# Optimization experiments

Measured on AMD Instinct MI355X. Metric: run time of the kernel, lower is better.

The kernel has to match this reference:

```python
import jax, jax.numpy as jnp
import numpy as np
jax.config.update("jax_enable_x64", True)

K = 10            # num_digits
NUM_CLASSES = 10  # digit classes 0..9
EQ_TOKEN = 28
PRIMES = np.array([7, 11, 13, 17, 19, 23, 29, 31, 37], dtype=np.int64)
TWO_PI = 2.0 * np.pi
M_TOTAL = int(np.prod(PRIMES.astype(object)))  # product of primes ~2.47e11 (needs int64)
_crt = []
for p in PRIMES:
    Mi = M_TOTAL // int(p)
    _crt.append((Mi * pow(Mi, -1, int(p))) % M_TOTAL)
CRT_C = jnp.array(_crt, dtype=jnp.int64)                 # [P] CRT mixing coefficients
POW10 = jnp.array([[pow(10, k, int(p)) for k in range(K)] for p in PRIMES], dtype=jnp.float32)  # [P,K]
PR_F = jnp.array(PRIMES, dtype=jnp.float32)
PR_I = jnp.array(PRIMES, dtype=jnp.int64)
POW10_DEC = jnp.array([10 ** k for k in range(K)], dtype=jnp.int64)
_op = np.full(64, -1, dtype=np.int64)
_op[20:25] = np.arange(5)  # tokens 20..24 -> ops add,sub,mul,exp,div
OP_TABLE = jnp.array(_op)


def encode(d):
    # d [B,S,K] soft base-10 digits -> RNS circle encoding [B,S,P,2]
    theta = TWO_PI * jnp.einsum('bsk,pk->bsp', d, POW10) / PR_F
    return jnp.stack([jnp.cos(theta), jnp.sin(theta)], axis=-1)


def decode_residues(circle):
    # [B,S,P,2] -> integer residues mod p, [B,S,P] int64
    theta = jnp.arctan2(circle[..., 1], circle[..., 0])
    r = jnp.round(theta / TWO_PI * PR_F).astype(jnp.int64)
    return jnp.mod(r, PR_I)


def circle_add(a, b):
    ca, sa = a[..., 0], a[..., 1]
    cb, sb = b[..., 0], b[..., 1]
    return jnp.stack([ca * cb - sa * sb, sa * cb + ca * sb], axis=-1)


def circle_sub(a, b):
    ca, sa = a[..., 0], a[..., 1]
    cb, sb = b[..., 0], b[..., 1]
    return jnp.stack([ca * cb + sa * sb, sa * cb - ca * sb], axis=-1)


def modpow(base, exp, mod):
    # elementwise modular exponentiation, exponents < 64 (6 square-and-multiply steps)
    res = jnp.ones_like(base)
    b = jnp.mod(base, mod)
    e = exp
    for _ in range(6):
        res = jnp.where((e & 1) == 1, (res * b) % mod, res)
        b = (b * b) % mod
        e = e >> 1
    return res


def crt(residues):
    # CRT reconstruction: [B,S,P] -> [B,S] int64 in [0, M_TOTAL)
    return jnp.mod(jnp.sum(residues * CRT_C, axis=-1), M_TOTAL)


def crt_signed(residues):
    n = crt(residues)
    return jnp.where(n > M_TOTAL // 2, n - M_TOTAL, n)


def int_to_digits(n):
    # [B,S] int64 -> [B,S,K] float base-10 digits, LSB-first
    return ((n[..., None] // POW10_DEC) % 10).astype(jnp.float32)


def int_to_digits_signed(n):
    sign = (n < 0).astype(jnp.float32)[..., None]
    return jnp.concatenate([int_to_digits(jnp.abs(n)), sign], axis=-1)  # [B,S,K+1]


def decode_all_ops(a_c, b_c):
    # All 5 operations decoded to digit vectors -> [B,S,5K+1]
    ra = decode_residues(a_c)
    rb = decode_residues(b_c)
    add_d = int_to_digits(crt(decode_residues(circle_add(a_c, b_c))))
    sub_d = int_to_digits_signed(crt_signed(decode_residues(circle_sub(a_c, b_c))))
    mul_d = int_to_digits(crt((ra * rb) % PR_I))
    exp_d = int_to_digits(crt(modpow(ra, rb, PR_I)))
    inv = modpow(rb, PR_I - 2, PR_I)  # Fermat inverse
    div_r = jnp.where(rb == 0, 0, (ra * inv) % PR_I)
    div_d = int_to_digits(crt(div_r))
    return jnp.concatenate([add_d, sub_d, mul_d, exp_d, div_d], axis=-1)


def select_op(results, input_ids):
    # [B,S,5K+1] -> [B,S,K+1]: pick the relevant operation per sequence
    B, S, _ = results.shape
    pad = jnp.zeros((B, S, 1), results.dtype)
    ops = jnp.stack([
        jnp.concatenate([results[..., 0:K], pad], -1),
        results[..., K:2 * K + 1],
        jnp.concatenate([results[..., 2 * K + 1:3 * K + 1], pad], -1),
        jnp.concatenate([results[..., 3 * K + 1:4 * K + 1], pad], -1),
        jnp.concatenate([results[..., 4 * K + 1:5 * K + 1], pad], -1),
    ], axis=-2)  # [B,S,5,K+1]
    is_op = OP_TABLE[jnp.clip(input_ids, 0, 63)] >= 0
    op_pos = jnp.argmax(is_op, axis=1)  # first operator position per sequence
    op_tok = jnp.take_along_axis(input_ids, op_pos[:, None], axis=1)[:, 0]
    op_idx = OP_TABLE[jnp.clip(op_tok, 0, 63)]
    gidx = jnp.broadcast_to(jnp.clip(op_idx, 0, 4)[:, None, None, None], (B, S, 1, K + 1))
    sel = jnp.take_along_axis(ops, gidx, axis=-2)[..., 0, :]
    valid = (op_idx >= 0).astype(results.dtype)[:, None, None]
    return sel * valid


def reorder_msb(res):
    # LSB-first digits -> MSB-first, -1 sentinel past the last significant digit
    digits = res[..., :K]
    sign = res[..., K:]
    idx = jnp.arange(K)
    nz = digits != 0
    highest = jnp.max(jnp.where(nz, idx, -1), axis=-1)
    num_sig = jnp.where(jnp.any(nz, axis=-1), highest + 1, 1)
    src = jnp.clip(num_sig[..., None] - 1 - idx, 0, K - 1)
    msb = jnp.take_along_axis(digits, src, axis=-1)
    msb = jnp.where(idx < num_sig[..., None], msb, -1.0)
    return jnp.concatenate([msb, sign], axis=-1)


def setup_inputs() -> dict:
    key = jax.random.key(0)
    ks = jax.random.split(key, 6)
    B, S, D, MH = 16, 2048, 768, 128
    h = jax.random.normal(ks[0], (B, S, D), dtype=jnp.float32)
    input_ids = jax.random.randint(ks[1], (B, S), 0, 50, dtype=jnp.int64)
    W1 = jax.random.normal(ks[2], (D, MH), dtype=jnp.float32) * 0.02
    b1 = jnp.zeros((MH,), jnp.float32)
    W2 = jax.random.normal(ks[3], (MH, 2 * K * NUM_CLASSES), dtype=jnp.float32) * 0.02
    b2 = jnp.zeros((2 * K * NUM_CLASSES,), jnp.float32)
    Winj = jax.random.normal(ks[4], (K + 1, D), dtype=jnp.float32) * 0.001  # injector_init_std
    binj = jnp.zeros((D,), jnp.float32)
    gate_logit = jnp.array(-2.0, jnp.float32)  # gate_init_logit
    return {"h": h, "W1": W1, "b1": b1, "W2": W2, "b2": b2,
            "Winj": Winj, "binj": binj, "gate_logit": gate_logit, "input_ids": input_ids}


def reference(h, W1, b1, W2, b2, Winj, binj, gate_logit, input_ids):
    B, S, D = h.shape
    # OperandExtractor: per-token MLP -> soft digits for operands a and b
    hid = jax.nn.relu(h @ W1 + b1)
    logits = (hid @ W2 + b2).reshape(B, S, 2, K, NUM_CLASSES)
    probs = jax.nn.softmax(logits, axis=-1)
    dig = jnp.einsum('bsokc,c->bsok', probs, jnp.arange(NUM_CLASSES, dtype=h.dtype))
    d_a, d_b = dig[..., 0, :], dig[..., 1, :]
    # RNSCircleEncoder (frozen)
    a_c = encode(d_a)
    b_c = encode(d_b)
    # ArithmeticCompute + CRT decode: detached (torch.no_grad in original)
    results = jax.lax.stop_gradient(decode_all_ops(a_c, b_c).astype(h.dtype))
    sel = select_op(results, input_ids)
    msb = reorder_msb(sel)
    # ResultInjector: gated linear injection into the residual stream
    inj = msb @ Winj + binj
    h_prime = h + jax.nn.sigmoid(gate_logit) * inj
    # only inject for sequences containing the '=' token
    has_eq = jnp.any(input_ids == EQ_TOKEN, axis=1).astype(h.dtype)[:, None, None]
    h_prime = h + (h_prime - h) * has_eq
    return h_prime, d_a, d_b
```

## Files before the change

kernel.cpp:

```cpp
#include <hip/hip_runtime.h>

typedef unsigned short u16;
typedef unsigned int   u32;
typedef unsigned long long u64;

typedef __attribute__((ext_vector_type(8))) short short8;
typedef __attribute__((ext_vector_type(4))) float f32x4;

#define DEV static __device__ __forceinline__

__constant__ float POW10F[9][10] = {
  {1,3,2,6,4,5,1,3,2,6},
  {1,10,1,10,1,10,1,10,1,10},
  {1,10,9,12,3,4,1,10,9,12},
  {1,10,15,14,4,6,9,5,16,7},
  {1,10,5,12,6,3,11,15,17,18},
  {1,10,8,11,18,19,6,14,2,20},
  {1,10,13,14,24,8,22,17,25,18},
  {1,10,7,8,18,25,2,20,14,16},
  {1,10,26,1,10,26,1,10,26,1},
};

#define M_TOTAL  247357937827ull
#define M_HALF   123678968913ull

DEV u16 f2bf_rne(float f){
  u32 u = __float_as_uint(f);
  return (u16)((u + 0x7FFFu + ((u >> 16) & 1u)) >> 16);
}
DEV float bf2f(u16 v){ return __uint_as_float(((u32)v) << 16); }

DEV short8 pack_bf16(float4 a, float4 b){
  union { short8 s; u32 u[4]; } r;
  r.u[0] = (__float_as_uint(a.x) >> 16) | (__float_as_uint(a.y) & 0xFFFF0000u);
  r.u[1] = (__float_as_uint(a.z) >> 16) | (__float_as_uint(a.w) & 0xFFFF0000u);
  r.u[2] = (__float_as_uint(b.x) >> 16) | (__float_as_uint(b.y) & 0xFFFF0000u);
  r.u[3] = (__float_as_uint(b.z) >> 16) | (__float_as_uint(b.w) & 0xFFFF0000u);
  return r.s;
}

DEV void load_lds16(const void* g, void* l){
  __builtin_amdgcn_global_load_lds((const __attribute__((address_space(1))) void*)g,
                                   (__attribute__((address_space(3))) void*)l, 16, 0, 0);
}

DEV int modpow6(int b, int e, int p){
  int res = 1; b %= p;
  #pragma unroll
  for (int i = 0; i < 6; ++i){
    if (e & 1) res = (res * b) % p;
    b = (b * b) % p;
    e >>= 1;
  }
  return res;
}

__global__ void prelude_kernel(const int* __restrict__ ids, const float* __restrict__ W1,
                               const float* __restrict__ W2, int* __restrict__ op_idx,
                               float* __restrict__ has_eq, u16* __restrict__ w1f,
                               u16* __restrict__ w2f){
  __shared__ int smin[256];
  __shared__ int seq[256];
  int bid = blockIdx.x, tid = threadIdx.x;
  if (bid < 16){
    int b = bid;
    int best = 2048, eq = 0;
    for (int i = tid; i < 2048; i += 256){
      int t = ids[b * 2048 + i];
      if (t >= 20 && t < 25) best = min(best, i);
      eq |= (t == 28) ? 1 : 0;
    }
    smin[tid] = best; seq[tid] = eq;
    __syncthreads();
    for (int s = 128; s > 0; s >>= 1){
      if (tid < s){ smin[tid] = min(smin[tid], smin[tid + s]); seq[tid] |= seq[tid + s]; }
      __syncthreads();
    }
    if (tid == 0){
      int op = -1;
      if (smin[0] < 2048) op = ids[b * 2048 + smin[0]] - 20;
      op_idx[b] = op;
      has_eq[b] = seq[0] ? 1.0f : 0.0f;
    }
  } else {
    int t = (bid - 16) * 256 + tid;
    if (t < 12288){
      int blk = t >> 6, L = t & 63;
      int T = blk >> 3, b = blk & 7;
      int q = L >> 4, ln = L & 15;
      #pragma unroll
      for (int j = 0; j < 8; ++j){
        int k = 32 * T + 8 * q + j;
        int n = 16 * b + ln;
        w1f[(size_t)blk * 512 + L * 8 + j] = f2bf_rne(W1[k * 128 + n]);
      }
    } else {
      int t2 = t - 12288;
      int blk = t2 >> 6, L = t2 & 63;
      int ts = blk / 13, b2 = blk % 13;
      int q = L >> 4, ln = L & 15;
      #pragma unroll
      for (int j = 0; j < 8; ++j){
        int k = 32 * ts + 8 * q + j;
        int n = 16 * b2 + ln;
        w2f[(size_t)blk * 512 + L * 8 + j] = (n < 200) ? f2bf_rne(W2[k * 200 + n]) : (u16)0;
      }
    }
  }
}

__launch_bounds__(256, 2)
__global__ void mega_kernel(const float* __restrict__ h, const u16* __restrict__ w1f,
                            const u16* __restrict__ w2f, const float* __restrict__ b1,
                            const float* __restrict__ b2, const float* __restrict__ Winj,
                            const float* __restrict__ binj, const float* __restrict__ gate,
                            const int* __restrict__ op_idx_ws, const float* __restrict__ has_eq_ws,
                            float* __restrict__ dout){
  __shared__ __align__(16) char lds[49152];
  u16*   wbuf     = (u16*)lds;
  char*  tail     = lds + 32768;
  float* digits_s = (float*)tail;
  float* tab_s    = (float*)(tail + 5120);
  u64*   ops_s    = (u64*)(tail + 9728);
  float* msbv     = (float*)(tail + 12288);
  u16*   hidf     = (u16*)tail;
  float* winj_s   = (float*)lds;
  float* binj_s   = (float*)(lds + 33792);

  const int tid  = threadIdx.x;
  const int w    = tid >> 6;
  const int lane = tid & 63;
  const int ln   = lane & 15, q = lane >> 4;
  const int wg   = blockIdx.x;
  const int tok0 = wg * 64;
  const int gtok = tok0 + w * 16 + ln;
  const int batch = wg >> 5;

  const int   op = op_idx_ws[batch];
  const float G  = has_eq_ws[batch] * (1.0f / (1.0f + __expf(-gate[0])));

  float b1v[8];
  #pragma unroll
  for (int b = 0; b < 8; ++b) b1v[b] = b1[ln + 16 * b];
  float b2v[13];
  #pragma unroll
  for (int b = 0; b < 13; ++b){ int n = ln + 16 * b; b2v[b] = (n < 200) ? b2[n] : 0.0f; }

  f32x4 acc[8];
  #pragma unroll
  for (int b = 0; b < 8; ++b) acc[b] = (f32x4)0.0f;

  const float4* ap = (const float4*)(h + (size_t)gtok * 768);
  float4 xa[2], xb[2];
  #pragma unroll
  for (int i = 0; i < 4; ++i){
    int bl = w * 4 + i;
    load_lds16(w1f + (size_t)(((bl >> 3)) * 8 + (bl & 7)) * 512 + lane * 8,
               wbuf + bl * 512);
  }
  #pragma unroll
  for (int t = 0; t < 2; ++t){ xa[t] = ap[t * 8 + q * 2]; xb[t] = ap[t * 8 + q * 2 + 1]; }

  #pragma unroll
  for (int c = 0; c < 12; ++c){
    __syncthreads();
    const u16* cur = wbuf + (c & 1) * 8192;
    if (c < 11){
      u16* nxt = wbuf + ((c + 1) & 1) * 8192;
      #pragma unroll
      for (int i = 0; i < 4; ++i){
        int bl = w * 4 + i;
        int T  = (c + 1) * 2 + (bl >> 3);
        load_lds16(w1f + (size_t)(T * 8 + (bl & 7)) * 512 + lane * 8, nxt + bl * 512);
      }
    }
    short8 af[2];
    #pragma unroll
    for (int t = 0; t < 2; ++t) af[t] = pack_bf16(xa[t], xb[t]);
    if (c < 11){
      const float4* ap2 = ap + (c + 1) * 16;
      #pragma unroll
      for (int t = 0; t < 2; ++t){ xa[t] = ap2[t * 8 + q * 2]; xb[t] = ap2[t * 8 + q * 2 + 1]; }
    }
    #pragma unroll
    for (int t = 0; t < 2; ++t){
      #pragma unroll
      for (int b = 0; b < 8; ++b){
        short8 bf = *(const short8*)(cur + (t * 8 + b) * 512 + lane * 8);
        acc[b] = __builtin_amdgcn_mfma_f32_16x16x32_bf16(af[t], bf, acc[b], 0, 0, 0);
      }
    }
  }

  #pragma unroll
  for (int b = 0; b < 8; ++b){
    int t2 = b >> 1;
    int q2 = ((b & 1) << 1) | (ln >> 3);
    int j  = ln & 7;
    #pragma unroll
    for (int r = 0; r < 4; ++r){
      float v = fmaxf(acc[b][r] + b1v[b], 0.0f);
      int L2 = (q2 << 4) | (q * 4 + r);
      hidf[w * 2048 + t2 * 512 + L2 * 8 + j] = (u16)(__float_as_uint(v) >> 16);
    }
  }
  __syncthreads();

  short8 a2[4];
  #pragma unroll
  for (int t = 0; t < 4; ++t) a2[t] = *(const short8*)(hidf + w * 2048 + t * 512 + lane * 8);
  f32x4 acc2[13];
  #pragma unroll
  for (int b = 0; b < 13; ++b) acc2[b] = (f32x4)0.0f;
  #pragma unroll
  for (int b = 0; b < 13; ++b){
    #pragma unroll
    for (int t = 0; t < 4; ++t){
      short8 bf = *(const short8*)(w2f + (size_t)(t * 13 + b) * 512 + lane * 8);
      acc2[b] = __builtin_amdgcn_mfma_f32_16x16x32_bf16(a2[t], bf, acc2[b], 0, 0, 0);
    }
  }

  #pragma unroll
  for (int b = 0; b < 13; ++b){
    #pragma unroll
    for (int r = 0; r < 4; ++r){
      float v = acc2[b][r] + b2v[b];
      wbuf[w * 4096 + (q * 4 + r) * 212 + ln + 16 * b] = (u16)(__float_as_uint(v) >> 16);
    }
  }
  __syncthreads();

  #pragma unroll
  for (int i = 0; i < 5; ++i){
    int task = tid + i * 256;
    int tok = task / 20, slot = task % 20;
    const u16* lp = wbuf + (tok >> 4) * 4096 + (tok & 15) * 212 + slot * 10;
    float v[10];
    #pragma unroll
    for (int k = 0; k < 10; ++k) v[k] = bf2f(lp[k]);
    float mx = v[0];
    #pragma unroll
    for (int k = 1; k < 10; ++k) mx = fmaxf(mx, v[k]);
    float s = 0.0f, sd = 0.0f;
    #pragma unroll
    for (int k = 0; k < 10; ++k){
      float e = __expf(v[k] - mx);
      s += e; sd += e * (float)k;
    }
    float dig = sd / s;
    digits_s[tok * 20 + slot] = dig;
    int gt = tok0 + tok;
    int o = slot / 10, k10 = slot % 10;
    dout[(size_t)25165824 + (size_t)o * 327680 + (size_t)gt * 10 + k10] = dig;
  }
  __syncthreads();

  #pragma unroll
  for (int i = 0; i < 8; ++i){
    int idx = tid + i * 256;
    float4 vsrc = *(const float4*)(Winj + (size_t)idx * 4);
    *(float4*)(winj_s + (size_t)idx * 4) = vsrc;
  }

  #pragma unroll
  for (int i = 0; i < 5; ++i){
    int task = tid + i * 256;
    if (task < 1152){
      int tok = task / 18, rm = task % 18;
      int ab = rm / 9, pi = rm % 9;
      float t = 0.0f;
      #pragma unroll
      for (int k = 0; k < 10; ++k) t += digits_s[tok * 20 + ab * 10 + k] * POW10F[pi][k];
      tab_s[tok * 18 + ab * 9 + pi] = t;
    }
  }
  __syncthreads();

  {
    int idx = 2048 + (tid >> 1) + ((tid & 1) ? 224 : 0);
  }
  if (tid < 224){
    #pragma unroll
    for (int i = 0; i < 2; ++i){
      int idx = 2048 + tid + i * 224;
      if (idx < 2496){
        const float* src = (idx < 2112) ? (Winj + (size_t)idx * 4)
                                        : (binj + (size_t)(idx - 2112) * 4);
        float4 vsrc = *(const float4*)src;
        *(float4*)(winj_s + (size_t)idx * 4) = vsrc;
      }
    }
  }

  {
    constexpr int PR[9] = {7, 11, 13, 17, 19, 23, 29, 31, 37};
    constexpr u64 CRTC[9] = {
      35336848261ull, 224870852570ull, 114165202074ull, 218257003965ull,
      78113032998ull, 53773464745ull, 68236672504ull, 223420072876ull, 220616539143ull
    };
    #pragma unroll
    for (int rep = 0; rep < 2; ++rep){
      int task = tid + rep * 256;
      if (task < 320){
        int o5 = task >> 6, tok = task & 63;
        u64 acc64 = 0;
        #pragma unroll
        for (int pi = 0; pi < 9; ++pi){
          const int p = PR[pi];
          float ta = tab_s[tok * 18 + pi], tb = tab_s[tok * 18 + 9 + pi];
          int r;
          if (o5 == 0){
            r = __float2int_rn(ta + tb) % p;
          } else if (o5 == 1){
            int s = __float2int_rn(ta - tb) % p;
            r = (s < 0) ? s + p : s;
          } else {
            int ra = __float2int_rn(ta) % p;
            int rb = __float2int_rn(tb) % p;
            if (o5 == 2) r = (ra * rb) % p;
            else if (o5 == 3) r = modpow6(ra, rb, p);
            else r = (rb == 0) ? 0 : (ra * modpow6(rb, p - 2, p)) % p;
          }
          acc64 += (u64)r * CRTC[pi];
        }
        u64 n = acc64 % M_TOTAL;
        int sign = 0;
        u64 un = n;
        if (o5 == 1 && n > M_HALF){ sign = 1; un = M_TOTAL - n; }
        u64 pk = 0;
        #pragma unroll
        for (int k = 0; k < 10; ++k){ pk |= (un % 10ull) << (4 * k); un /= 10ull; }
        pk |= ((u64)sign) << 40;
        ops_s[tok * 5 + o5] = pk;
      }
    }
  }
  __syncthreads();

  if (tid < 64){
    int tok = tid;
    u64 pk = (op >= 0) ? ops_s[tok * 5 + op] : 0ull;
    int g[10]; int hi = -1;
    #pragma unroll
    for (int k = 0; k < 10; ++k){
      g[k] = (int)((pk >> (4 * k)) & 15ull);
      if (g[k] != 0) hi = k;
    }
    int ns = (hi >= 0) ? hi + 1 : 1;
    #pragma unroll
    for (int i = 0; i < 10; ++i)
      msbv[tok * 12 + i] = (i < ns) ? (float)g[ns - 1 - i] : -1.0f;
    msbv[tok * 12 + 10] = (float)((pk >> 40) & 1ull);
    msbv[tok * 12 + 11] = 0.0f;
  }
  __syncthreads();

  if (tid < 192){
    float4 wv[11];
    #pragma unroll
    for (int j = 0; j < 11; ++j) wv[j] = *(const float4*)(winj_s + j * 768 + tid * 4);
    float4 bj = *(const float4*)(binj_s + tid * 4);
    const size_t base = (size_t)tok0 * 768 + tid * 4;
    #pragma unroll 4
    for (int tt = 0; tt < 64; ++tt){
      float4 m0 = *(const float4*)(msbv + tt * 12);
      float4 m1 = *(const float4*)(msbv + tt * 12 + 4);
      float4 m2 = *(const float4*)(msbv + tt * 12 + 8);
      float4 hv = *(const float4*)(h + base + (size_t)tt * 768);
      float ix = bj.x, iy = bj.y, iz = bj.z, iw = bj.w;
      ix += m0.x*wv[0].x + m0.y*wv[1].x + m0.z*wv[2].x + m0.w*wv[3].x
          + m1.x*wv[4].x + m1.y*wv[5].x + m1.z*wv[6].x + m1.w*wv[7].x
          + m2.x*wv[8].x + m2.y*wv[9].x + m2.z*wv[10].x;
      iy += m0.x*wv[0].y + m0.y*wv[1].y + m0.z*wv[2].y + m0.w*wv[3].y
          + m1.x*wv[4].y + m1.y*wv[5].y + m1.z*wv[6].y + m1.w*wv[7].y
          + m2.x*wv[8].y + m2.y*wv[9].y + m2.z*wv[10].y;
      iz += m0.x*wv[0].z + m0.y*wv[1].z + m0.z*wv[2].z + m0.w*wv[3].z
          + m1.x*wv[4].z + m1.y*wv[5].z + m1.z*wv[6].z + m1.w*wv[7].z
          + m2.x*wv[8].z + m2.y*wv[9].z + m2.z*wv[10].z;
      iw += m0.x*wv[0].w + m0.y*wv[1].w + m0.z*wv[2].w + m0.w*wv[3].w
          + m1.x*wv[4].w + m1.y*wv[5].w + m1.z*wv[6].w + m1.w*wv[7].w
          + m2.x*wv[8].w + m2.y*wv[9].w + m2.z*wv[10].w;
      float4 o;
      o.x = hv.x + G * ix; o.y = hv.y + G * iy;
      o.z = hv.z + G * iz; o.w = hv.w + G * iw;
      *(float4*)(dout + base + (size_t)tt * 768) = o;
    }
  }
}

extern "C" void kernel_launch(void* const* d_in, const int* in_sizes, int n_in,
                              void* d_out, int out_size, void* d_ws, size_t ws_size,
                              hipStream_t stream){
  const float* h    = (const float*)d_in[0];
  const float* W1   = (const float*)d_in[1];
  const float* b1   = (const float*)d_in[2];
  const float* W2   = (const float*)d_in[3];
  const float* b2   = (const float*)d_in[4];
  const float* Winj = (const float*)d_in[5];
  const float* binj = (const float*)d_in[6];
  const float* gate = (const float*)d_in[7];
  const int*   ids  = (const int*)d_in[8];
  float* dout = (float*)d_out;

  char* ws = (char*)d_ws;
  int*   op_idx = (int*)(ws + 0);
  float* has_eq = (float*)(ws + 64);
  u16*   w1f    = (u16*)(ws + 256);
  u16*   w2f    = (u16*)(ws + 256 + 196608);

  prelude_kernel<<<77, 256, 0, stream>>>(ids, W1, W2, op_idx, has_eq, w1f, w2f);
  mega_kernel<<<512, 256, 0, stream>>>(h, w1f, w2f, b1, b2, Winj, binj, gate,
                                       op_idx, has_eq, dout);
}
```

Before: 232.0 us.

## Halve tokens per workgroup and split GEMM N-dimension across wave pairs

Each workgroup now handles 32 tokens instead of 64, with four waves arranged as 2 token-rows by 2 N-halves for both MLP GEMMs. The grid doubles to 1024 blocks, LDS shrinks to 40KB, and launch bounds target 4 blocks per SM, all aimed at more parallelism and occupancy. Winj and binj are now read straight from global memory instead of being staged in LDS. In exchange, every W1 chunk is streamed from global memory twice as often per token, and per-block fixed overhead is repeated across twice as many blocks.

```diff
diff --git a/kernel.cpp b/kernel.cpp
--- a/kernel.cpp
+++ b/kernel.cpp
@@ -109,46 +109,43 @@
   }
 }
 
-__launch_bounds__(256, 2)
+__launch_bounds__(256, 4)
 __global__ void mega_kernel(const float* __restrict__ h, const u16* __restrict__ w1f,
                             const u16* __restrict__ w2f, const float* __restrict__ b1,
                             const float* __restrict__ b2, const float* __restrict__ Winj,
                             const float* __restrict__ binj, const float* __restrict__ gate,
                             const int* __restrict__ op_idx_ws, const float* __restrict__ has_eq_ws,
                             float* __restrict__ dout){
-  __shared__ __align__(16) char lds[49152];
+  __shared__ __align__(16) char lds[40960];
   u16*   wbuf     = (u16*)lds;
   char*  tail     = lds + 32768;
+  u16*   hidf     = (u16*)tail;
   float* digits_s = (float*)tail;
-  float* tab_s    = (float*)(tail + 5120);
-  u64*   ops_s    = (u64*)(tail + 9728);
-  float* msbv     = (float*)(tail + 12288);
-  u16*   hidf     = (u16*)tail;
-  float* winj_s   = (float*)lds;
-  float* binj_s   = (float*)(lds + 33792);
+  float* tab_s    = (float*)(tail + 2560);
+  u64*   ops_s    = (u64*)(tail + 4864);
+  float* msbv     = (float*)(tail + 6144);
 
   const int tid  = threadIdx.x;
   const int w    = tid >> 6;
   const int lane = tid & 63;
   const int ln   = lane & 15, q = lane >> 4;
+  const int m    = w & 1;
+  const int nh   = w >> 1;
   const int wg   = blockIdx.x;
-  const int tok0 = wg * 64;
-  const int gtok = tok0 + w * 16 + ln;
-  const int batch = wg >> 5;
+  const int tok0 = wg * 32;
+  const int gtok = tok0 + m * 16 + ln;
+  const int batch = wg >> 6;
 
   const int   op = op_idx_ws[batch];
   const float G  = has_eq_ws[batch] * (1.0f / (1.0f + __expf(-gate[0])));
 
-  float b1v[8];
-  #pragma unroll
-  for (int b = 0; b < 8; ++b) b1v[b] = b1[ln + 16 * b];
-  float b2v[13];
-  #pragma unroll
-  for (int b = 0; b < 13; ++b){ int n = ln + 16 * b; b2v[b] = (n < 200) ? b2[n] : 0.0f; }
-
-  f32x4 acc[8];
-  #pragma unroll
-  for (int b = 0; b < 8; ++b) acc[b] = (f32x4)0.0f;
+  float b1v[4];
+  #pragma unroll
+  for (int b = 0; b < 4; ++b) b1v[b] = b1[nh * 64 + 16 * b + ln];
+
+  f32x4 acc[4];
+  #pragma unroll
+  for (int b = 0; b < 4; ++b) acc[b] = (f32x4)0.0f;
 
   const float4* ap = (const float4*)(h + (size_t)gtok * 768);
   float4 xa[2], xb[2];
@@ -185,88 +182,97 @@
     #pragma unroll
     for (int t = 0; t < 2; ++t){
       #pragma unroll
-      for (int b = 0; b < 8; ++b){
-        short8 bf = *(const short8*)(cur + (t * 8 + b) * 512 + lane * 8);
+      for (int b = 0; b < 4; ++b){
+        short8 bf = *(const short8*)(cur + (t * 8 + nh * 4 + b) * 512 + lane * 8);
         acc[b] = __builtin_amdgcn_mfma_f32_16x16x32_bf16(af[t], bf, acc[b], 0, 0, 0);
       }
     }
   }
 
   #pragma unroll
-  for (int b = 0; b < 8; ++b){
-    int t2 = b >> 1;
-    int q2 = ((b & 1) << 1) | (ln >> 3);
+  for (int b = 0; b < 4; ++b){
+    int nb = nh * 4 + b;
+    int t2 = nb >> 1;
+    int q2 = ((nb & 1) << 1) | (ln >> 3);
     int j  = ln & 7;
     #pragma unroll
     for (int r = 0; r < 4; ++r){
       float v = fmaxf(acc[b][r] + b1v[b], 0.0f);
       int L2 = (q2 << 4) | (q * 4 + r);
-      hidf[w * 2048 + t2 * 512 + L2 * 8 + j] = (u16)(__float_as_uint(v) >> 16);
+      hidf[m * 2048 + t2 * 512 + L2 * 8 + j] = (u16)(__float_as_uint(v) >> 16);
     }
   }
   __syncthreads();
 
   short8 a2[4];
   #pragma unroll
-  for (int t = 0; t < 4; ++t) a2[t] = *(const short8*)(hidf + w * 2048 + t * 512 + lane * 8);
-  f32x4 acc2[13];
-  #pragma unroll
-  for (int b = 0; b < 13; ++b) acc2[b] = (f32x4)0.0f;
-  #pragma unroll
-  for (int b = 0; b < 13; ++b){
-    #pragma unroll
-    for (int t = 0; t < 4; ++t){
-      short8 bf = *(const short8*)(w2f + (size_t)(t * 13 + b) * 512 + lane * 8);
-      acc2[b] = __builtin_amdgcn_mfma_f32_16x16x32_bf16(a2[t], bf, acc2[b], 0, 0, 0);
-    }
-  }
-
-  #pragma unroll
-  for (int b = 0; b < 13; ++b){
-    #pragma unroll
-    for (int r = 0; r < 4; ++r){
-      float v = acc2[b][r] + b2v[b];
-      wbuf[w * 4096 + (q * 4 + r) * 212 + ln + 16 * b] = (u16)(__float_as_uint(v) >> 16);
-    }
-  }
-  __syncthreads();
-
-  #pragma unroll
-  for (int i = 0; i < 5; ++i){
+  for (int t = 0; t < 4; ++t) a2[t] = *(const short8*)(hidf + m * 2048 + t * 512 + lane * 8);
+  const int nb2 = 7 - nh;
+  float b2v[7];
+  #pragma unroll
+  for (int bb = 0; bb < 7; ++bb){
+    int n = (nh * 7 + bb) * 16 + ln;
+    b2v[bb] = (bb < nb2 && n < 200) ? b2[n] : 0.0f;
+  }
+  f32x4 acc2[7];
+  #pragma unroll
+  for (int bb = 0; bb < 7; ++bb) acc2[bb] = (f32x4)0.0f;
+  #pragma unroll
+  for (int bb = 0; bb < 7; ++bb){
+    if (bb < nb2){
+      #pragma unroll
+      for (int t = 0; t < 4; ++t){
+        short8 bf = *(const short8*)(w2f + (size_t)(t * 13 + nh * 7 + bb) * 512 + lane * 8);
+        acc2[bb] = __builtin_amdgcn_mfma_f32_16x16x32_bf16(a2[t], bf, acc2[bb], 0, 0, 0);
+      }
+    }
+  }
+
+  #pragma unroll
+  for (int bb = 0; bb < 7; ++bb){
+    if (bb < nb2){
+      #pragma unroll
+      for (int r = 0; r < 4; ++r){
+        float v = acc2[bb][r] + b2v[bb];
+        int tk = m * 16 + q * 4 + r;
+        int n  = (nh * 7 + bb) * 16 + ln;
+        wbuf[tk * 212 + n] = (u16)(__float_as_uint(v) >> 16);
+      }
+    }
+  }
+  __syncthreads();
+
+  #pragma unroll
+  for (int i = 0; i < 3; ++i){
     int task = tid + i * 256;
-    int tok = task / 20, slot = task % 20;
-    const u16* lp = wbuf + (tok >> 4) * 4096 + (tok & 15) * 212 + slot * 10;
-    float v[10];
-    #pragma unroll
-    for (int k = 0; k < 10; ++k) v[k] = bf2f(lp[k]);
-    float mx = v[0];
-    #pragma unroll
-    for (int k = 1; k < 10; ++k) mx = fmaxf(mx, v[k]);
-    float s = 0.0f, sd = 0.0f;
-    #pragma unroll
-    for (int k = 0; k < 10; ++k){
-      float e = __expf(v[k] - mx);
-      s += e; sd += e * (float)k;
-    }
-    float dig = sd / s;
-    digits_s[tok * 20 + slot] = dig;
-    int gt = tok0 + tok;
-    int o = slot / 10, k10 = slot % 10;
-    dout[(size_t)25165824 + (size_t)o * 327680 + (size_t)gt * 10 + k10] = dig;
-  }
-  __syncthreads();
-
-  #pragma unroll
-  for (int i = 0; i < 8; ++i){
-    int idx = tid + i * 256;
-    float4 vsrc = *(const float4*)(Winj + (size_t)idx * 4);
-    *(float4*)(winj_s + (size_t)idx * 4) = vsrc;
-  }
-
-  #pragma unroll
-  for (int i = 0; i < 5; ++i){
+    if (task < 640){
+      int tok = task / 20, slot = task % 20;
+      const u16* lp = wbuf + tok * 212 + slot * 10;
+      float v[10];
+      #pragma unroll
+      for (int k = 0; k < 10; ++k) v[k] = bf2f(lp[k]);
+      float mx = v[0];
+      #pragma unroll
+      for (int k = 1; k < 10; ++k) mx = fmaxf(mx, v[k]);
+      float s = 0.0f, sd = 0.0f;
+      #pragma unroll
+      for (int k = 0; k < 10; ++k){
+        float e = __expf(v[k] - mx);
+        s += e; sd += e * (float)k;
+      }
+      float dig = sd / s;
+      digits_s[tok * 20 + slot] = dig;
+      int gt = tok0 + tok;
+      int o = slot / 10, k10 = slot % 10;
+      dout[(size_t)25165824 + (size_t)o * 327680 + (size_t)gt * 10 + k10] = dig;
+    }
+  }
+  __syncthreads();
+
+  #pragma unroll
+  for (int i = 0; i < 3; ++i){
     int task = tid + i * 256;
-    if (task < 1152){
+    if (task < 576){
       int tok = task / 18, rm = task % 18;
       int ab = rm / 9, pi = rm % 9;
       float t = 0.0f;
@@ -276,22 +282,6 @@
     }
   }
   __syncthreads();
-
-  {
-    int idx = 2048 + (tid >> 1) + ((tid & 1) ? 224 : 0);
-  }
-  if (tid < 224){
-    #pragma unroll
-    for (int i = 0; i < 2; ++i){
-      int idx = 2048 + tid + i * 224;
-      if (idx < 2496){
-        const float* src = (idx < 2112) ? (Winj + (size_t)idx * 4)
-                                        : (binj + (size_t)(idx - 2112) * 4);
-        float4 vsrc = *(const float4*)src;
-        *(float4*)(winj_s + (size_t)idx * 4) = vsrc;
-      }
-    }
-  }
 
   {
     constexpr int PR[9] = {7, 11, 13, 17, 19, 23, 29, 31, 37};
@@ -299,46 +289,42 @@
       35336848261ull, 224870852570ull, 114165202074ull, 218257003965ull,
       78113032998ull, 53773464745ull, 68236672504ull, 223420072876ull, 220616539143ull
     };
-    #pragma unroll
-    for (int rep = 0; rep < 2; ++rep){
-      int task = tid + rep * 256;
-      if (task < 320){
-        int o5 = task >> 6, tok = task & 63;
-        u64 acc64 = 0;
-        #pragma unroll
-        for (int pi = 0; pi < 9; ++pi){
-          const int p = PR[pi];
-          float ta = tab_s[tok * 18 + pi], tb = tab_s[tok * 18 + 9 + pi];
-          int r;
-          if (o5 == 0){
-            r = __float2int_rn(ta + tb) % p;
-          } else if (o5 == 1){
-            int s = __float2int_rn(ta - tb) % p;
-            r = (s < 0) ? s + p : s;
-          } else {
-            int ra = __float2int_rn(ta) % p;
-            int rb = __float2int_rn(tb) % p;
-            if (o5 == 2) r = (ra * rb) % p;
-            else if (o5 == 3) r = modpow6(ra, rb, p);
-            else r = (rb == 0) ? 0 : (ra * modpow6(rb, p - 2, p)) % p;
-          }
-          acc64 += (u64)r * CRTC[pi];
+    if (tid < 160){
+      int o5 = tid >> 5, tok = tid & 31;
+      u64 acc64 = 0;
+      #pragma unroll
+      for (int pi = 0; pi < 9; ++pi){
+        const int p = PR[pi];
+        float ta = tab_s[tok * 18 + pi], tb = tab_s[tok * 18 + 9 + pi];
+        int r;
+        if (o5 == 0){
+          r = __float2int_rn(ta + tb) % p;
+        } else if (o5 == 1){
+          int s = __float2int_rn(ta - tb) % p;
+          r = (s < 0) ? s + p : s;
+        } else {
+          int ra = __float2int_rn(ta) % p;
+          int rb = __float2int_rn(tb) % p;
+          if (o5 == 2) r = (ra * rb) % p;
+          else if (o5 == 3) r = modpow6(ra, rb, p);
+          else r = (rb == 0) ? 0 : (ra * modpow6(rb, p - 2, p)) % p;
         }
-        u64 n = acc64 % M_TOTAL;
-        int sign = 0;
-        u64 un = n;
-        if (o5 == 1 && n > M_HALF){ sign = 1; un = M_TOTAL - n; }
-        u64 pk = 0;
-        #pragma unroll
-        for (int k = 0; k < 10; ++k){ pk |= (un % 10ull) << (4 * k); un /= 10ull; }
-        pk |= ((u64)sign) << 40;
-        ops_s[tok * 5 + o5] = pk;
-      }
-    }
-  }
-  __syncthreads();
-
-  if (tid < 64){
+        acc64 += (u64)r * CRTC[pi];
+      }
+      u64 n = acc64 % M_TOTAL;
+      int sign = 0;
+      u64 un = n;
+      if (o5 == 1 && n > M_HALF){ sign = 1; un = M_TOTAL - n; }
+      u64 pk = 0;
+      #pragma unroll
+      for (int k = 0; k < 10; ++k){ pk |= (un % 10ull) << (4 * k); un /= 10ull; }
+      pk |= ((u64)sign) << 40;
+      ops_s[tok * 5 + o5] = pk;
+    }
+  }
+  __syncthreads();
+
+  if (tid < 32){
     int tok = tid;
     u64 pk = (op >= 0) ? ops_s[tok * 5 + op] : 0ull;
     int g[10]; int hi = -1;
@@ -359,11 +345,11 @@
   if (tid < 192){
     float4 wv[11];
     #pragma unroll
-    for (int j = 0; j < 11; ++j) wv[j] = *(const float4*)(winj_s + j * 768 + tid * 4);
-    float4 bj = *(const float4*)(binj_s + tid * 4);
+    for (int j = 0; j < 11; ++j) wv[j] = *(const float4*)(Winj + (size_t)j * 768 + tid * 4);
+    float4 bj = *(const float4*)(binj + tid * 4);
     const size_t base = (size_t)tok0 * 768 + tid * 4;
     #pragma unroll 4
-    for (int tt = 0; tt < 64; ++tt){
+    for (int tt = 0; tt < 32; ++tt){
       float4 m0 = *(const float4*)(msbv + tt * 12);
       float4 m1 = *(const float4*)(msbv + tt * 12 + 4);
       float4 m2 = *(const float4*)(msbv + tt * 12 + 8);
@@ -410,6 +396,6 @@
   u16*   w2f    = (u16*)(ws + 256 + 196608);
 
   prelude_kernel<<<77, 256, 0, stream>>>(ids, W1, W2, op_idx, has_eq, w1f, w2f);
-  mega_kernel<<<512, 256, 0, stream>>>(h, w1f, w2f, b1, b2, Winj, binj, gate,
-                                       op_idx, has_eq, dout);
-}
+  mega_kernel<<<1024, 256, 0, stream>>>(h, w1f, w2f, b1, b2, Winj, binj, gate,
+                                        op_idx, has_eq, dout);
+}
```

Result: slower. 322.7 us (+39.1%).

## Make mega_kernel wave-independent, drop LDS staging of W1 and block barriers

Applied to the files above, without the earlier changes.

Each wave now runs the whole pipeline on its own 16 tokens in a private LDS slice, and every block-wide __syncthreads becomes a wave-local lgkmcnt wait. The W1 bf16 fragments are read straight from global memory (expected to hit L2) instead of being double-buffered into LDS with global_load_lds. Winj and binj are also read directly rather than staged. LDS per block drops from 48KB to 32KB, and removing cross-wave barriers should let waves drift apart. The cost is that each wave re-reads W1 and Winj from global/L2 with no cross-wave sharing in LDS.

```diff
diff --git a/kernel.cpp b/kernel.cpp
--- a/kernel.cpp
+++ b/kernel.cpp
@@ -39,11 +39,6 @@
   return r.s;
 }
 
-DEV void load_lds16(const void* g, void* l){
-  __builtin_amdgcn_global_load_lds((const __attribute__((address_space(1))) void*)g,
-                                   (__attribute__((address_space(3))) void*)l, 16, 0, 0);
-}
-
 DEV int modpow6(int b, int e, int p){
   int res = 1; b %= p;
   #pragma unroll
@@ -54,6 +49,11 @@
   }
   return res;
 }
+
+#define WAVE_SYNC() do { \
+  asm volatile("s_waitcnt lgkmcnt(0)" ::: "memory"); \
+  __builtin_amdgcn_sched_barrier(0); \
+} while (0)
 
 __global__ void prelude_kernel(const int* __restrict__ ids, const float* __restrict__ W1,
                                const float* __restrict__ W2, int* __restrict__ op_idx,
@@ -116,16 +116,7 @@
                             const float* __restrict__ binj, const float* __restrict__ gate,
                             const int* __restrict__ op_idx_ws, const float* __restrict__ has_eq_ws,
                             float* __restrict__ dout){
-  __shared__ __align__(16) char lds[49152];
-  u16*   wbuf     = (u16*)lds;
-  char*  tail     = lds + 32768;
-  float* digits_s = (float*)tail;
-  float* tab_s    = (float*)(tail + 5120);
-  u64*   ops_s    = (u64*)(tail + 9728);
-  float* msbv     = (float*)(tail + 12288);
-  u16*   hidf     = (u16*)tail;
-  float* winj_s   = (float*)lds;
-  float* binj_s   = (float*)(lds + 33792);
+  __shared__ __align__(16) char lds[32768];
 
   const int tid  = threadIdx.x;
   const int w    = tid >> 6;
@@ -133,47 +124,35 @@
   const int ln   = lane & 15, q = lane >> 4;
   const int wg   = blockIdx.x;
   const int tok0 = wg * 64;
-  const int gtok = tok0 + w * 16 + ln;
+  const int wtok0 = tok0 + w * 16;
   const int batch = wg >> 5;
 
   const int   op = op_idx_ws[batch];
   const float G  = has_eq_ws[batch] * (1.0f / (1.0f + __expf(-gate[0])));
 
+  char*  wls      = lds + (w << 13);
+  u16*   hidf     = (u16*)wls;
+  u16*   logit    = (u16*)wls;
+  float* digits_s = (float*)(wls + 6784);
+  float* tab_s    = (float*)wls;
+  u64*   ops_s    = (u64*)(wls + 1536);
+  float* msbv     = (float*)(wls + 2560);
+
   float b1v[8];
   #pragma unroll
   for (int b = 0; b < 8; ++b) b1v[b] = b1[ln + 16 * b];
-  float b2v[13];
-  #pragma unroll
-  for (int b = 0; b < 13; ++b){ int n = ln + 16 * b; b2v[b] = (n < 200) ? b2[n] : 0.0f; }
 
   f32x4 acc[8];
   #pragma unroll
   for (int b = 0; b < 8; ++b) acc[b] = (f32x4)0.0f;
 
-  const float4* ap = (const float4*)(h + (size_t)gtok * 768);
+  const float4* ap = (const float4*)(h + (size_t)(wtok0 + ln) * 768);
   float4 xa[2], xb[2];
   #pragma unroll
-  for (int i = 0; i < 4; ++i){
-    int bl = w * 4 + i;
-    load_lds16(w1f + (size_t)(((bl >> 3)) * 8 + (bl & 7)) * 512 + lane * 8,
-               wbuf + bl * 512);
-  }
-  #pragma unroll
   for (int t = 0; t < 2; ++t){ xa[t] = ap[t * 8 + q * 2]; xb[t] = ap[t * 8 + q * 2 + 1]; }
 
   #pragma unroll
   for (int c = 0; c < 12; ++c){
-    __syncthreads();
-    const u16* cur = wbuf + (c & 1) * 8192;
-    if (c < 11){
-      u16* nxt = wbuf + ((c + 1) & 1) * 8192;
-      #pragma unroll
-      for (int i = 0; i < 4; ++i){
-        int bl = w * 4 + i;
-        int T  = (c + 1) * 2 + (bl >> 3);
-        load_lds16(w1f + (size_t)(T * 8 + (bl & 7)) * 512 + lane * 8, nxt + bl * 512);
-      }
-    }
     short8 af[2];
     #pragma unroll
     for (int t = 0; t < 2; ++t) af[t] = pack_bf16(xa[t], xb[t]);
@@ -186,7 +165,7 @@
     for (int t = 0; t < 2; ++t){
       #pragma unroll
       for (int b = 0; b < 8; ++b){
-        short8 bf = *(const short8*)(cur + (t * 8 + b) * 512 + lane * 8);
+        short8 bf = *(const short8*)(w1f + (size_t)(((c * 2 + t) * 8 + b)) * 512 + lane * 8);
         acc[b] = __builtin_amdgcn_mfma_f32_16x16x32_bf16(af[t], bf, acc[b], 0, 0, 0);
       }
     }
@@ -201,14 +180,19 @@
     for (int r = 0; r < 4; ++r){
       float v = fmaxf(acc[b][r] + b1v[b], 0.0f);
       int L2 = (q2 << 4) | (q * 4 + r);
-      hidf[w * 2048 + t2 * 512 + L2 * 8 + j] = (u16)(__float_as_uint(v) >> 16);
-    }
-  }
-  __syncthreads();
+      hidf[t2 * 512 + L2 * 8 + j] = (u16)(__float_as_uint(v) >> 16);
+    }
+  }
+  WAVE_SYNC();
 
   short8 a2[4];
   #pragma unroll
-  for (int t = 0; t < 4; ++t) a2[t] = *(const short8*)(hidf + w * 2048 + t * 512 + lane * 8);
+  for (int t = 0; t < 4; ++t) a2[t] = *(const short8*)(hidf + t * 512 + lane * 8);
+  WAVE_SYNC();
+
+  float b2v[13];
+  #pragma unroll
+  for (int b = 0; b < 13; ++b){ int n = ln + 16 * b; b2v[b] = (n < 200) ? b2[n] : 0.0f; }
   f32x4 acc2[13];
   #pragma unroll
   for (int b = 0; b < 13; ++b) acc2[b] = (f32x4)0.0f;
@@ -226,16 +210,16 @@
     #pragma unroll
     for (int r = 0; r < 4; ++r){
       float v = acc2[b][r] + b2v[b];
-      wbuf[w * 4096 + (q * 4 + r) * 212 + ln + 16 * b] = (u16)(__float_as_uint(v) >> 16);
-    }
-  }
-  __syncthreads();
+      logit[(q * 4 + r) * 212 + 16 * b + ln] = (u16)(__float_as_uint(v) >> 16);
+    }
+  }
+  WAVE_SYNC();
 
   #pragma unroll
   for (int i = 0; i < 5; ++i){
-    int task = tid + i * 256;
+    int task = i * 64 + lane;
     int tok = task / 20, slot = task % 20;
-    const u16* lp = wbuf + (tok >> 4) * 4096 + (tok & 15) * 212 + slot * 10;
+    const u16* lp = logit + tok * 212 + slot * 10;
     float v[10];
     #pragma unroll
     for (int k = 0; k < 10; ++k) v[k] = bf2f(lp[k]);
@@ -250,23 +234,16 @@
     }
     float dig = sd / s;
     digits_s[tok * 20 + slot] = dig;
-    int gt = tok0 + tok;
+    int gt = wtok0 + tok;
     int o = slot / 10, k10 = slot % 10;
     dout[(size_t)25165824 + (size_t)o * 327680 + (size_t)gt * 10 + k10] = dig;
   }
-  __syncthreads();
-
-  #pragma unroll
-  for (int i = 0; i < 8; ++i){
-    int idx = tid + i * 256;
-    float4 vsrc = *(const float4*)(Winj + (size_t)idx * 4);
-    *(float4*)(winj_s + (size_t)idx * 4) = vsrc;
-  }
+  WAVE_SYNC();
 
   #pragma unroll
   for (int i = 0; i < 5; ++i){
-    int task = tid + i * 256;
-    if (task < 1152){
+    int task = i * 64 + lane;
+    if (task < 288){
       int tok = task / 18, rm = task % 18;
       int ab = rm / 9, pi = rm % 9;
       float t = 0.0f;
@@ -275,23 +252,7 @@
       tab_s[tok * 18 + ab * 9 + pi] = t;
     }
   }
-  __syncthreads();
-
-  {
-    int idx = 2048 + (tid >> 1) + ((tid & 1) ? 224 : 0);
-  }
-  if (tid < 224){
-    #pragma unroll
-    for (int i = 0; i < 2; ++i){
-      int idx = 2048 + tid + i * 224;
-      if (idx < 2496){
-        const float* src = (idx < 2112) ? (Winj + (size_t)idx * 4)
-                                        : (binj + (size_t)(idx - 2112) * 4);
-        float4 vsrc = *(const float4*)src;
-        *(float4*)(winj_s + (size_t)idx * 4) = vsrc;
-      }
-    }
-  }
+  WAVE_SYNC();
 
   {
     constexpr int PR[9] = {7, 11, 13, 17, 19, 23, 29, 31, 37};
@@ -300,10 +261,10 @@
       78113032998ull, 53773464745ull, 68236672504ull, 223420072876ull, 220616539143ull
     };
     #pragma unroll
-    for (int rep = 0; rep < 2; ++rep){
-      int task = tid + rep * 256;
-      if (task < 320){
-        int o5 = task >> 6, tok = task & 63;
+    for (int i = 0; i < 2; ++i){
+      int task = i * 64 + lane;
+      if (task < 80){
+        int o5 = task >> 4, tok = task & 15;
         u64 acc64 = 0;
         #pragma unroll
         for (int pi = 0; pi < 9; ++pi){
@@ -336,10 +297,10 @@
       }
     }
   }
-  __syncthreads();
-
-  if (tid < 64){
-    int tok = tid;
+  WAVE_SYNC();
+
+  if (lane < 16){
+    int tok = lane;
     u64 pk = (op >= 0) ? ops_s[tok * 5 + op] : 0ull;
     int g[10]; int hi = -1;
     #pragma unroll
@@ -354,37 +315,43 @@
     msbv[tok * 12 + 10] = (float)((pk >> 40) & 1ull);
     msbv[tok * 12 + 11] = 0.0f;
   }
-  __syncthreads();
-
-  if (tid < 192){
-    float4 wv[11];
-    #pragma unroll
-    for (int j = 0; j < 11; ++j) wv[j] = *(const float4*)(winj_s + j * 768 + tid * 4);
-    float4 bj = *(const float4*)(binj_s + tid * 4);
-    const size_t base = (size_t)tok0 * 768 + tid * 4;
-    #pragma unroll 4
-    for (int tt = 0; tt < 64; ++tt){
-      float4 m0 = *(const float4*)(msbv + tt * 12);
-      float4 m1 = *(const float4*)(msbv + tt * 12 + 4);
-      float4 m2 = *(const float4*)(msbv + tt * 12 + 8);
-      float4 hv = *(const float4*)(h + base + (size_t)tt * 768);
-      float ix = bj.x, iy = bj.y, iz = bj.z, iw = bj.w;
-      ix += m0.x*wv[0].x + m0.y*wv[1].x + m0.z*wv[2].x + m0.w*wv[3].x
-          + m1.x*wv[4].x + m1.y*wv[5].x + m1.z*wv[6].x + m1.w*wv[7].x
-          + m2.x*wv[8].x + m2.y*wv[9].x + m2.z*wv[10].x;
-      iy += m0.x*wv[0].y + m0.y*wv[1].y + m0.z*wv[2].y + m0.w*wv[3].y
-          + m1.x*wv[4].y + m1.y*wv[5].y + m1.z*wv[6].y + m1.w*wv[7].y
-          + m2.x*wv[8].y + m2.y*wv[9].y + m2.z*wv[10].y;
-      iz += m0.x*wv[0].z + m0.y*wv[1].z + m0.z*wv[2].z + m0.w*wv[3].z
-          + m1.x*wv[4].z + m1.y*wv[5].z + m1.z*wv[6].z + m1.w*wv[7].z
-          + m2.x*wv[8].z + m2.y*wv[9].z + m2.z*wv[10].z;
-      iw += m0.x*wv[0].w + m0.y*wv[1].w + m0.z*wv[2].w + m0.w*wv[3].w
-          + m1.x*wv[4].w + m1.y*wv[5].w + m1.z*wv[6].w + m1.w*wv[7].w
-          + m2.x*wv[8].w + m2.y*wv[9].w + m2.z*wv[10].w;
-      float4 o;
-      o.x = hv.x + G * ix; o.y = hv.y + G * iy;
-      o.z = hv.z + G * iz; o.w = hv.w + G * iw;
-      *(float4*)(dout + base + (size_t)tt * 768) = o;
+  WAVE_SYNC();
+
+  {
+    const float4* Wj4 = (const float4*)Winj;
+    const float4* bj4 = (const float4*)binj;
+    #pragma unroll
+    for (int cc = 0; cc < 3; ++cc){
+      const int f = cc * 64 + lane;
+      float4 wv[11];
+      #pragma unroll
+      for (int j = 0; j < 11; ++j) wv[j] = Wj4[j * 192 + f];
+      float4 bj = bj4[f];
+      const size_t base = (size_t)wtok0 * 768 + (size_t)f * 4;
+      #pragma unroll 4
+      for (int row = 0; row < 16; ++row){
+        float4 m0 = *(const float4*)(msbv + row * 12);
+        float4 m1 = *(const float4*)(msbv + row * 12 + 4);
+        float4 m2 = *(const float4*)(msbv + row * 12 + 8);
+        float4 hv = *(const float4*)(h + base + (size_t)row * 768);
+        float ix = bj.x, iy = bj.y, iz = bj.z, iw = bj.w;
+        ix += m0.x*wv[0].x + m0.y*wv[1].x + m0.z*wv[2].x + m0.w*wv[3].x
+            + m1.x*wv[4].x + m1.y*wv[5].x + m1.z*wv[6].x + m1.w*wv[7].x
+            + m2.x*wv[8].x + m2.y*wv[9].x + m2.z*wv[10].x;
+        iy += m0.x*wv[0].y + m0.y*wv[1].y + m0.z*wv[2].y + m0.w*wv[3].y
+            + m1.x*wv[4].y + m1.y*wv[5].y + m1.z*wv[6].y + m1.w*wv[7].y
+            + m2.x*wv[8].y + m2.y*wv[9].y + m2.z*wv[10].y;
+        iz += m0.x*wv[0].z + m0.y*wv[1].z + m0.z*wv[2].z + m0.w*wv[3].z
+            + m1.x*wv[4].z + m1.y*wv[5].z + m1.z*wv[6].z + m1.w*wv[7].z
+            + m2.x*wv[8].z + m2.y*wv[9].z + m2.z*wv[10].z;
+        iw += m0.x*wv[0].w + m0.y*wv[1].w + m0.z*wv[2].w + m0.w*wv[3].w
+            + m1.x*wv[4].w + m1.y*wv[5].w + m1.z*wv[6].w + m1.w*wv[7].w
+            + m2.x*wv[8].w + m2.y*wv[9].w + m2.z*wv[10].w;
+        float4 o;
+        o.x = hv.x + G * ix; o.y = hv.y + G * iy;
+        o.z = hv.z + G * iz; o.w = hv.w + G * iw;
+        *(float4*)(dout + base + (size_t)row * 768) = o;
+      }
     }
   }
 }
```

Result: slower. 240.1 us (+3.5%).
